# Kernel tuning notes

Measured on AMD Instinct MI355X. Metric: run time of the kernel, lower is better.

## Reference

```python
import jax, jax.numpy as jnp
import numpy as np

B, S, E = 4, 2048, 512
H = 8
DK = E // H          # 64
NQ = 8               # n_qubits


def setup_inputs() -> dict:
    key = jax.random.key(0)
    ks = jax.random.split(key, 10)
    s = 1.0 / np.sqrt(E)
    return {
        "x": jax.random.normal(ks[0], (B, S, E), dtype=jnp.float32),
        "Wq": jax.random.normal(ks[1], (E, E), dtype=jnp.float32) * s,
        "bq": jnp.zeros((E,), dtype=jnp.float32),
        "Wk": jax.random.normal(ks[2], (E, E), dtype=jnp.float32) * s,
        "bk": jnp.zeros((E,), dtype=jnp.float32),
        "Wv": jax.random.normal(ks[3], (E, E), dtype=jnp.float32) * s,
        "bv": jnp.zeros((E,), dtype=jnp.float32),
        "Wo": jax.random.normal(ks[4], (E, E), dtype=jnp.float32) * s,
        "bo": jnp.zeros((E,), dtype=jnp.float32),
        "kernel_params": jax.random.normal(ks[5], (NQ, NQ), dtype=jnp.float32),
    }


def _split_heads(t):
    # [B,S,E] -> [B,H,S,DK]
    return t.reshape(B, S, H, DK).transpose(0, 2, 1, 3)


def reference(x, Wq, bq, Wk, bk, Wv, bv, Wo, bo, kernel_params):
    q = _split_heads(x @ Wq + bq)
    k = _split_heads(x @ Wk + bk)
    v = _split_heads(x @ Wv + bv)

    # Quantum kernel closed form: RX(x_i) then RZ(theta_ii) on wire i, measure <Z_i>.
    # RZ commutes with Z so <Z_i> = cos(x_i). Only the first NQ features are encoded.
    q_meas = jnp.cos(q[..., :NQ])  # [B,H,S,NQ]
    k_meas = jnp.cos(k[..., :NQ])  # [B,H,S,NQ]

    sim = jnp.einsum('bhqd,bhkd->bhqk', q_meas, k_meas)  # [B,H,S,S]
    attn = jax.nn.softmax(sim, axis=-1)
    out = jnp.einsum('bhqk,bhkd->bhqd', attn, v)          # [B,H,S,DK]
    out = out.transpose(0, 2, 1, 3).reshape(B, S, E)      # compose heads
    return out @ Wo + bo
```

## Files before the change

kernel.cpp:

```cpp
#include <hip/hip_runtime.h>
#include <hip/hip_bf16.h>

#define BB 4
#define SS 2048
#define EE 512
#define HH 8
#define DKK 64
#define NQQ 8
#define BS (BB * SS)

typedef __attribute__((ext_vector_type(4))) float f32x4;
typedef __attribute__((ext_vector_type(16))) float f32x16;
typedef _Float16 f16x8 __attribute__((ext_vector_type(8)));
typedef unsigned short u16;
typedef unsigned int u32;

union U4H8 { uint4 u; f16x8 h; };

__device__ __forceinline__ u16 f2h(float f) {
    _Float16 hv = (_Float16)f;
    return *reinterpret_cast<u16*>(&hv);
}
__device__ __forceinline__ float h2f(u16 u) {
    _Float16 h = *reinterpret_cast<_Float16*>(&u);
    return (float)h;
}

__global__ __launch_bounds__(256) void cvt2_kernel(
    const float4* __restrict__ in, uint2* __restrict__ xh, uint2* __restrict__ xl, int n4)
{
    int i = blockIdx.x * 256 + threadIdx.x;
    if (i >= n4) return;
    float4 a = in[i];
    u16 h0 = f2h(a.x), h1 = f2h(a.y), h2 = f2h(a.z), h3 = f2h(a.w);
    u16 l0 = f2h(a.x - h2f(h0)), l1 = f2h(a.y - h2f(h1));
    u16 l2 = f2h(a.z - h2f(h2)), l3 = f2h(a.w - h2f(h3));
    xh[i] = make_uint2((u32)h0 | ((u32)h1 << 16), (u32)h2 | ((u32)h3 << 16));
    xl[i] = make_uint2((u32)l0 | ((u32)l1 << 16), (u32)l2 | ((u32)l3 << 16));
}

__global__ __launch_bounds__(256) void wqk_pack_kernel(
    const float* __restrict__ Wq, const float* __restrict__ Wk,
    u16* __restrict__ Wh)
{
    const int n = blockIdx.x;
    const int col = (((n & 63) >> 3) << 6) | (n & 7);
    const float* src = (n < 64) ? Wq : Wk;
    for (int k = threadIdx.x; k < EE; k += 256) {
        Wh[(size_t)n * EE + k] = f2h(src[(size_t)k * EE + col]);
    }
}

__global__ __launch_bounds__(256) void wtrans_kernel(
    const float* __restrict__ W, u16* __restrict__ WT)
{
    __shared__ float ts[64][65];
    const int kt0 = blockIdx.x * 64, nt0 = blockIdx.y * 64;
    const int tid = threadIdx.x;
    #pragma unroll
    for (int i = 0; i < 4; ++i) {
        int c = tid + i * 256;
        int kr = c >> 4, nc = (c & 15) * 4;
        float4 t = *reinterpret_cast<const float4*>(&W[(size_t)(kt0 + kr) * EE + nt0 + nc]);
        ts[kr][nc] = t.x; ts[kr][nc + 1] = t.y; ts[kr][nc + 2] = t.z; ts[kr][nc + 3] = t.w;
    }
    __syncthreads();
    const int n = tid >> 2, k0 = (tid & 3) * 16;
    u32 o[8];
    #pragma unroll
    for (int j = 0; j < 8; ++j) {
        o[j] = (u32)f2h(ts[k0 + 2 * j][n]) | ((u32)f2h(ts[k0 + 2 * j + 1][n]) << 16);
    }
    uint4* dst = reinterpret_cast<uint4*>(&WT[(size_t)(nt0 + n) * EE + kt0 + k0]);
    dst[0] = make_uint4(o[0], o[1], o[2], o[3]);
    dst[1] = make_uint4(o[4], o[5], o[6], o[7]);
}

__global__ __launch_bounds__(256) void qk_mfma_kernel(
    const u16* __restrict__ xh, const u16* __restrict__ xl,
    const u16* __restrict__ Wh,
    const float* __restrict__ bq, const float* __restrict__ bk,
    u16* __restrict__ qf, u16* __restrict__ kf)
{
    __shared__ u16 Asl[64 * 64];
    __shared__ u16 Bsl[64 * 64];

    const int tid = threadIdx.x;
    const int lane = tid & 63;
    const int ww = tid >> 6;
    const int wr = ww >> 1, wc = ww & 1;
    const int tx = lane & 15, tyq = lane >> 4;
    const int m0 = blockIdx.x * 64;
    const int isK = blockIdx.y;
    const int nbase = isK * 64;

    const int c0 = tid, c1 = tid + 256;
    const int r0 = c0 >> 3, o0 = (c0 & 7) * 8, d0 = r0 * 64 + (((c0 & 7) ^ (r0 & 7)) * 8);
    const int r1 = c1 >> 3, o1 = (c1 & 7) * 8, d1 = r1 * 64 + (((c1 & 7) ^ (r1 & 7)) * 8);

    uint4 pa0, pa1, pb0, pb1;
    auto ldi = [&](int it) {
        int pass = it >> 3, k0 = (it & 7) * 64;
        const u16* Ab = pass ? xl : xh;
        pa0 = *reinterpret_cast<const uint4*>(&Ab[(size_t)(m0 + r0) * EE + k0 + o0]);
        pb0 = *reinterpret_cast<const uint4*>(&Wh[(size_t)(nbase + r0) * EE + k0 + o0]);
        pa1 = *reinterpret_cast<const uint4*>(&Ab[(size_t)(m0 + r1) * EE + k0 + o1]);
        pb1 = *reinterpret_cast<const uint4*>(&Wh[(size_t)(nbase + r1) * EE + k0 + o1]);
    };
    auto st = [&]() {
        *reinterpret_cast<uint4*>(&Asl[d0]) = pa0;
        *reinterpret_cast<uint4*>(&Bsl[d0]) = pb0;
        *reinterpret_cast<uint4*>(&Asl[d1]) = pa1;
        *reinterpret_cast<uint4*>(&Bsl[d1]) = pb1;
    };

    f32x4 acc[2][2];
    #pragma unroll
    for (int mt = 0; mt < 2; ++mt)
        #pragma unroll
        for (int nt = 0; nt < 2; ++nt) acc[mt][nt] = (f32x4)(0.f);

    const int bkx = tx & 7;
    ldi(0);
    for (int it = 0; it < 16; ++it) {
        __syncthreads();
        st();
        if (it < 15) ldi(it + 1);
        __syncthreads();
        #pragma unroll
        for (int kb = 0; kb < 2; ++kb) {
            f16x8 af[2], bfg[2];
            const int kblk = ((kb * 4 + tyq) ^ bkx) * 8;
            #pragma unroll
            for (int mt = 0; mt < 2; ++mt)
                af[mt] = *reinterpret_cast<const f16x8*>(&Asl[(wr * 32 + mt * 16 + tx) * 64 + kblk]);
            #pragma unroll
            for (int nt = 0; nt < 2; ++nt)
                bfg[nt] = *reinterpret_cast<const f16x8*>(&Bsl[(wc * 32 + nt * 16 + tx) * 64 + kblk]);
            #pragma unroll
            for (int mt = 0; mt < 2; ++mt)
                #pragma unroll
                for (int nt = 0; nt < 2; ++nt)
                    acc[mt][nt] = __builtin_amdgcn_mfma_f32_16x16x32_f16(
                        af[mt], bfg[nt], acc[mt][nt], 0, 0, 0);
        }
    }

    const float* bias = isK ? bk : bq;
    u16* dst = isK ? kf : qf;
    #pragma unroll
    for (int mt = 0; mt < 2; ++mt) {
        #pragma unroll
        for (int nt = 0; nt < 2; ++nt) {
            int nl = wc * 32 + nt * 16 + tx;
            int h = nl >> 3, f = nl & 7;
            float bcol = bias[h * 64 + f];
            #pragma unroll
            for (int r = 0; r < 4; ++r) {
                int s = m0 + wr * 32 + mt * 16 + tyq * 4 + r;
                float c = __cosf(acc[mt][nt][r] + bcol);
                size_t bh = (size_t)((s >> 11) * HH + h);
                dst[(bh * SS + (s & 2047)) * 8 + f] = f2h(c);
            }
        }
    }
}

template<int MODE>
__global__ __launch_bounds__(256) void mfma_gemm_kernel(
    const u16* __restrict__ A, const u16* __restrict__ Bm,
    const float* __restrict__ bias, float* __restrict__ outf, u16* __restrict__ outb)
{
    __shared__ u16 smem[8448];
    u16* Asl = smem;
    u16* Bsl = smem + 4096;

    const int tid = threadIdx.x;
    const int lane = tid & 63;
    const int ww = tid >> 6;
    const int wr = ww >> 1, wc = ww & 1;
    const int tx = lane & 15, tyq = lane >> 4;
    const int m0 = blockIdx.x * 64, n0 = blockIdx.y * 64;

    const int c0 = tid, c1 = tid + 256;
    const int r0 = c0 >> 3, o0 = (c0 & 7) * 8, d0 = r0 * 64 + (((c0 & 7) ^ (r0 & 7)) * 8);
    const int r1 = c1 >> 3, o1 = (c1 & 7) * 8, d1 = r1 * 64 + (((c1 & 7) ^ (r1 & 7)) * 8);

    uint4 pa0, pa1, pb0, pb1;
    auto ld = [&](int ks) {
        int k0 = ks * 64;
        pa0 = *reinterpret_cast<const uint4*>(&A [(size_t)(m0 + r0) * EE + k0 + o0]);
        pb0 = *reinterpret_cast<const uint4*>(&Bm[(size_t)(n0 + r0) * EE + k0 + o0]);
        pa1 = *reinterpret_cast<const uint4*>(&A [(size_t)(m0 + r1) * EE + k0 + o1]);
        pb1 = *reinterpret_cast<const uint4*>(&Bm[(size_t)(n0 + r1) * EE + k0 + o1]);
    };
    auto st = [&]() {
        *reinterpret_cast<uint4*>(&Asl[d0]) = pa0;
        *reinterpret_cast<uint4*>(&Bsl[d0]) = pb0;
        *reinterpret_cast<uint4*>(&Asl[d1]) = pa1;
        *reinterpret_cast<uint4*>(&Bsl[d1]) = pb1;
    };

    f32x4 acc[2][2];
    #pragma unroll
    for (int mt = 0; mt < 2; ++mt)
        #pragma unroll
        for (int nt = 0; nt < 2; ++nt) acc[mt][nt] = (f32x4)(0.f);

    const int bkx = tx & 7;
    ld(0);
    for (int ks = 0; ks < 8; ++ks) {
        __syncthreads();
        st();
        if (ks < 7) ld(ks + 1);
        __syncthreads();
        #pragma unroll
        for (int kb = 0; kb < 2; ++kb) {
            f16x8 af[2], bfg[2];
            const int kblk = ((kb * 4 + tyq) ^ bkx) * 8;
            #pragma unroll
            for (int mt = 0; mt < 2; ++mt)
                af[mt] = *reinterpret_cast<const f16x8*>(&Asl[(wr * 32 + mt * 16 + tx) * 64 + kblk]);
            #pragma unroll
            for (int nt = 0; nt < 2; ++nt)
                bfg[nt] = *reinterpret_cast<const f16x8*>(&Bsl[(wc * 32 + nt * 16 + tx) * 64 + kblk]);
            #pragma unroll
            for (int mt = 0; mt < 2; ++mt)
                #pragma unroll
                for (int nt = 0; nt < 2; ++nt)
                    acc[mt][nt] = __builtin_amdgcn_mfma_f32_16x16x32_f16(
                        af[mt], bfg[nt], acc[mt][nt], 0, 0, 0);
        }
    }

    if (MODE == 0) {
        #pragma unroll
        for (int mt = 0; mt < 2; ++mt) {
            #pragma unroll
            for (int nt = 0; nt < 2; ++nt) {
                int gcol = n0 + wc * 32 + nt * 16 + tx;
                float bcol = bias[gcol];
                #pragma unroll
                for (int r = 0; r < 4; ++r) {
                    int grow = m0 + wr * 32 + mt * 16 + tyq * 4 + r;
                    outf[(size_t)grow * EE + gcol] = acc[mt][nt][r] + bcol;
                }
            }
        }
    } else {
        __syncthreads();
        #pragma unroll
        for (int mt = 0; mt < 2; ++mt) {
            #pragma unroll
            for (int nt = 0; nt < 2; ++nt) {
                int kl = wc * 32 + nt * 16 + tx;
                #pragma unroll
                for (int r = 0; r < 4; ++r) {
                    int dl = wr * 32 + mt * 16 + tyq * 4 + r;
                    float vb = acc[mt][nt][r] + bias[m0 + dl];
                    smem[dl * 66 + kl] = f2h(vb);
                }
            }
        }
        __syncthreads();
        const size_t slab = (size_t)((n0 >> 11) * HH + (m0 >> 6)) * (SS * DKK);
        const int cell0 = (n0 & 2047) >> 3;
        #pragma unroll
        for (int i = 0; i < 2; ++i) {
            int item = tid + i * 256;
            int d = item & 63, ci = item >> 6;
            int kb = 16 * (ci >> 1) + 4 * (ci & 1);
            u16 g[8];
            #pragma unroll
            for (int j = 0; j < 8; ++j) {
                int klocal = kb + (j & 3) + 8 * (j >> 2);
                g[j] = smem[d * 66 + klocal];
            }
            uint4 p;
            p.x = (u32)g[0] | ((u32)g[1] << 16);
            p.y = (u32)g[2] | ((u32)g[3] << 16);
            p.z = (u32)g[4] | ((u32)g[5] << 16);
            p.w = (u32)g[6] | ((u32)g[7] << 16);
            *reinterpret_cast<uint4*>(&outb[slab + (size_t)(cell0 + ci) * 512 + d * 8]) = p;
        }
    }
}

__global__ __launch_bounds__(256, 4) void attn_v7_kernel(
    const u16* __restrict__ qf, const u16* __restrict__ kf,
    const u16* __restrict__ VT2, u16* __restrict__ attb)
{
    __shared__ float fsh[128 * 33];

    const int tid = threadIdx.x;
    const int lane = tid & 63;
    const int wv = tid >> 6;
    const int kslice = wv >> 1;
    const int qw = wv & 1;
    const int l31 = lane & 31;
    const int hi = lane >> 5;

    const int bid = blockIdx.x;
    const int xcd = bid & 7, sub = bid >> 3;
    const int bh = (xcd << 2) | (sub >> 5);
    const int q0 = (sub & 31) * 64;

    const u16* __restrict__ qfb = qf + (size_t)bh * SS * 8;
    const u16* __restrict__ kfb = kf + (size_t)bh * SS * 8;
    const u16* __restrict__ V2b = VT2 + (size_t)bh * SS * DKK;

    const uint4 z4 = make_uint4(0u, 0u, 0u, 0u);

    U4H8 qb;
    qb.u = hi ? z4 : *reinterpret_cast<const uint4*>(&qfb[(size_t)(q0 + qw * 32 + l31) * 8]);
    const f16x8 QB = qb.h;

    f32x16 acc0 = (f32x16)(0.f), acc1 = (f32x16)(0.f);
    float z = 0.f;

    const int ks_off = kslice * 1024;

    auto vld = [&](int t, int s, uint4* dst) {
        const int K0 = ks_off + t * 64 + s * 32;
        #pragma unroll
        for (int c = 0; c < 2; ++c) {
            const size_t cb = (size_t)((((K0 >> 4) + c) << 1) + hi) * 512;
            dst[c * 2]     = *reinterpret_cast<const uint4*>(&V2b[cb + l31 * 8]);
            dst[c * 2 + 1] = *reinterpret_cast<const uint4*>(&V2b[cb + (32 + l31) * 8]);
        }
    };

    U4H8 kc0, kc1, kn0, kn1;
    auto ldk = [&](int t, U4H8& a, U4H8& b) {
        int kt = ks_off + t * 64;
        a.u = hi ? z4 : *reinterpret_cast<const uint4*>(&kfb[(size_t)(kt + l31) * 8]);
        b.u = hi ? z4 : *reinterpret_cast<const uint4*>(&kfb[(size_t)(kt + 32 + l31) * 8]);
    };

    uint4 vA[4], vB[4];
    ldk(0, kc0, kc1);
    vld(0, 0, vA);

    for (int t = 0; t < 16; ++t) {
        vld(t, 1, vB);
        if (t < 15) ldk(t + 1, kn0, kn1);
        {
            f32x16 sim = (f32x16)(0.f);
            sim = __builtin_amdgcn_mfma_f32_32x32x16_f16(kc0.h, QB, sim, 0, 0, 0);
            float w[16];
            #pragma unroll
            for (int r = 0; r < 16; ++r) w[r] = __expf(sim[r]);
            float zp = 0.f;
            #pragma unroll
            for (int r = 0; r < 8; ++r) zp += (w[2 * r] + w[2 * r + 1]);
            z += zp;
            #pragma unroll
            for (int c = 0; c < 2; ++c) {
                f16x8 PA;
                #pragma unroll
                for (int j = 0; j < 8; ++j) PA[j] = (_Float16)w[8 * c + j];
                U4H8 b0, b1; b0.u = vA[c * 2]; b1.u = vA[c * 2 + 1];
                acc0 = __builtin_amdgcn_mfma_f32_32x32x16_f16(PA, b0.h, acc0, 0, 0, 0);
                acc1 = __builtin_amdgcn_mfma_f32_32x32x16_f16(PA, b1.h, acc1, 0, 0, 0);
            }
        }
        if (t < 15) vld(t + 1, 0, vA);
        {
            f32x16 sim = (f32x16)(0.f);
            sim = __builtin_amdgcn_mfma_f32_32x32x16_f16(kc1.h, QB, sim, 0, 0, 0);
            float w[16];
            #pragma unroll
            for (int r = 0; r < 16; ++r) w[r] = __expf(sim[r]);
            float zp = 0.f;
            #pragma unroll
            for (int r = 0; r < 8; ++r) zp += (w[2 * r] + w[2 * r + 1]);
            z += zp;
            #pragma unroll
            for (int c = 0; c < 2; ++c) {
                f16x8 PA;
                #pragma unroll
                for (int j = 0; j < 8; ++j) PA[j] = (_Float16)w[8 * c + j];
                U4H8 b0, b1; b0.u = vB[c * 2]; b1.u = vB[c * 2 + 1];
                acc0 = __builtin_amdgcn_mfma_f32_32x32x16_f16(PA, b0.h, acc0, 0, 0, 0);
                acc1 = __builtin_amdgcn_mfma_f32_32x32x16_f16(PA, b1.h, acc1, 0, 0, 0);
            }
        }
        kc0 = kn0; kc1 = kn1;
    }

    const int cbase = (qw * 64 + lane) * 33;
    if (kslice == 1) {
        #pragma unroll
        for (int r = 0; r < 16; ++r) {
            fsh[cbase + r] = acc0[r];
            fsh[cbase + 16 + r] = acc1[r];
        }
        fsh[cbase + 32] = z;
    }
    __syncthreads();
    if (kslice == 0) {
        #pragma unroll
        for (int r = 0; r < 16; ++r) {
            acc0[r] += fsh[cbase + r];
            acc1[r] += fsh[cbase + 16 + r];
        }
        z += fsh[cbase + 32];
        z += __shfl_xor(z, 32, 64);
        float zinv = 1.0f / z;

        const int b = bh >> 3, h = bh & 7;
        #pragma unroll
        for (int r = 0; r < 16; ++r) {
            int qrow = (r & 3) + 8 * (r >> 2) + 4 * hi;
            float zi = __shfl(zinv, qrow, 32);
            size_t base = ((size_t)b * SS + q0 + qw * 32 + qrow) * EE + h * DKK + l31;
            attb[base]      = f2h(acc0[r] * zi);
            attb[base + 32] = f2h(acc1[r] * zi);
        }
    }
}

extern "C" void kernel_launch(void* const* d_in, const int* in_sizes, int n_in,
                              void* d_out, int out_size, void* d_ws, size_t ws_size,
                              hipStream_t stream)
{
    const float* x  = (const float*)d_in[0];
    const float* Wq = (const float*)d_in[1];
    const float* bq = (const float*)d_in[2];
    const float* Wk = (const float*)d_in[3];
    const float* bk = (const float*)d_in[4];
    const float* Wv = (const float*)d_in[5];
    const float* bv = (const float*)d_in[6];
    const float* Wo = (const float*)d_in[7];
    const float* bo = (const float*)d_in[8];

    char* w = (char*)d_ws;
    u16* xh    = (u16*)w;  w += (size_t)BS * EE * 2;
    u16* xl    = (u16*)w;  w += (size_t)BS * EE * 2;
    u16* Wqk   = (u16*)w;  w += (size_t)128 * EE * 2;
    u16* WvT   = (u16*)w;  w += (size_t)EE * EE * 2;
    u16* WoT   = (u16*)w;  w += (size_t)EE * EE * 2;
    u16* qf    = (u16*)w;  w += (size_t)BB * HH * SS * 8 * 2;
    u16* kf    = (u16*)w;  w += (size_t)BB * HH * SS * 8 * 2;
    u16* VT2   = (u16*)w;  w += (size_t)BB * HH * DKK * SS * 2;
    u16* attb  = xl;
    float* out = (float*)d_out;

    cvt2_kernel<<<dim3(BS * EE / 4 / 256), 256, 0, stream>>>(
        (const float4*)x, (uint2*)xh, (uint2*)xl, BS * EE / 4);
    wqk_pack_kernel<<<dim3(128), 256, 0, stream>>>(Wq, Wk, Wqk);
    wtrans_kernel<<<dim3(8, 8), 256, 0, stream>>>(Wv, WvT);
    wtrans_kernel<<<dim3(8, 8), 256, 0, stream>>>(Wo, WoT);
    qk_mfma_kernel<<<dim3(BS / 64, 2), 256, 0, stream>>>(
        xh, xl, Wqk, bq, bk, qf, kf);
    mfma_gemm_kernel<1><<<dim3(EE / 64, BS / 64), 256, 0, stream>>>(
        WvT, xh, bv, nullptr, VT2);
    attn_v7_kernel<<<dim3(1024), 256, 0, stream>>>(qf, kf, VT2, attb);
    mfma_gemm_kernel<0><<<dim3(BS / 64, EE / 64), 256, 0, stream>>>(
        attb, WoT, bo, out, nullptr);
}
```

Measured before the change: 85.49 us.

## Give each attention wave both query tiles and split keys four ways

The attention kernel changes from 2 query-waves × 2 key-slices to 4 key-slices, where each wave handles all 64 query rows. Each loaded K and V fragment is now reused for two query tiles, which halves per-wave global loads of V. The final partial sums are combined with a two-stage shared-memory tree reduction. The f32-to-f16 conversion of the probabilities switches to packed cvt_pkrtz, and launch bounds drop to 3 waves/SIMD to make room for more accumulator registers. The cost is more registers, lower occupancy and extra syncthreads in the reduction.

After: 156.6 us. +83.2%, slower.

```diff
diff --git a/kernel.cpp b/kernel.cpp
--- a/kernel.cpp
+++ b/kernel.cpp
@@ -11,11 +11,13 @@
 
 typedef __attribute__((ext_vector_type(4))) float f32x4;
 typedef __attribute__((ext_vector_type(16))) float f32x16;
+typedef __fp16 fp16x2 __attribute__((ext_vector_type(2)));
 typedef _Float16 f16x8 __attribute__((ext_vector_type(8)));
 typedef unsigned short u16;
 typedef unsigned int u32;
 
 union U4H8 { uint4 u; f16x8 h; };
+union PK8 { fp16x2 p[4]; f16x8 h; };
 
 __device__ __forceinline__ u16 f2h(float f) {
     _Float16 hv = (_Float16)f;
@@ -286,17 +288,15 @@
     }
 }
 
-__global__ __launch_bounds__(256, 4) void attn_v7_kernel(
+__global__ __launch_bounds__(256, 3) void attn_v8_kernel(
     const u16* __restrict__ qf, const u16* __restrict__ kf,
     const u16* __restrict__ VT2, u16* __restrict__ attb)
 {
-    __shared__ float fsh[128 * 33];
+    __shared__ float fsh[2][64][67];
 
     const int tid = threadIdx.x;
     const int lane = tid & 63;
-    const int wv = tid >> 6;
-    const int kslice = wv >> 1;
-    const int qw = wv & 1;
+    const int ks = tid >> 6;
     const int l31 = lane & 31;
     const int hi = lane >> 5;
 
@@ -311,17 +311,20 @@
 
     const uint4 z4 = make_uint4(0u, 0u, 0u, 0u);
 
-    U4H8 qb;
-    qb.u = hi ? z4 : *reinterpret_cast<const uint4*>(&qfb[(size_t)(q0 + qw * 32 + l31) * 8]);
-    const f16x8 QB = qb.h;
-
-    f32x16 acc0 = (f32x16)(0.f), acc1 = (f32x16)(0.f);
-    float z = 0.f;
-
-    const int ks_off = kslice * 1024;
-
-    auto vld = [&](int t, int s, uint4* dst) {
-        const int K0 = ks_off + t * 64 + s * 32;
+    U4H8 qb0, qb1;
+    qb0.u = hi ? z4 : *reinterpret_cast<const uint4*>(&qfb[(size_t)(q0 + l31) * 8]);
+    qb1.u = hi ? z4 : *reinterpret_cast<const uint4*>(&qfb[(size_t)(q0 + 32 + l31) * 8]);
+    const f16x8 QB0 = qb0.h;
+    const f16x8 QB1 = qb1.h;
+
+    f32x16 acc00 = (f32x16)(0.f), acc01 = (f32x16)(0.f);
+    f32x16 acc10 = (f32x16)(0.f), acc11 = (f32x16)(0.f);
+    float z0 = 0.f, z1 = 0.f;
+
+    const int ks_off = ks * 512;
+
+    auto vld = [&](int t, uint4 (&dst)[4]) {
+        const int K0 = ks_off + t * 32;
         #pragma unroll
         for (int c = 0; c < 2; ++c) {
             const size_t cb = (size_t)((((K0 >> 4) + c) << 1) + hi) * 512;
@@ -329,93 +332,101 @@
             dst[c * 2 + 1] = *reinterpret_cast<const uint4*>(&V2b[cb + (32 + l31) * 8]);
         }
     };
-
-    U4H8 kc0, kc1, kn0, kn1;
-    auto ldk = [&](int t, U4H8& a, U4H8& b) {
-        int kt = ks_off + t * 64;
-        a.u = hi ? z4 : *reinterpret_cast<const uint4*>(&kfb[(size_t)(kt + l31) * 8]);
-        b.u = hi ? z4 : *reinterpret_cast<const uint4*>(&kfb[(size_t)(kt + 32 + l31) * 8]);
+    auto kld = [&](int t, U4H8& a) {
+        const int K0 = ks_off + t * 32;
+        a.u = hi ? z4 : *reinterpret_cast<const uint4*>(&kfb[(size_t)(K0 + l31) * 8]);
+    };
+
+    auto phase = [&](const U4H8& kc, const uint4 (&vv)[4]) {
+        f32x16 s0 = (f32x16)(0.f), s1 = (f32x16)(0.f);
+        s0 = __builtin_amdgcn_mfma_f32_32x32x16_f16(kc.h, QB0, s0, 0, 0, 0);
+        s1 = __builtin_amdgcn_mfma_f32_32x32x16_f16(kc.h, QB1, s1, 0, 0, 0);
+        float w0[16], w1[16];
+        #pragma unroll
+        for (int r = 0; r < 16; ++r) w0[r] = __expf(s0[r]);
+        #pragma unroll
+        for (int r = 0; r < 16; ++r) w1[r] = __expf(s1[r]);
+        float zp0 = 0.f, zp1 = 0.f;
+        #pragma unroll
+        for (int r = 0; r < 8; ++r) { zp0 += (w0[2*r] + w0[2*r+1]); zp1 += (w1[2*r] + w1[2*r+1]); }
+        z0 += zp0; z1 += zp1;
+        #pragma unroll
+        for (int c = 0; c < 2; ++c) {
+            PK8 pa0, pa1;
+            #pragma unroll
+            for (int j = 0; j < 4; ++j) {
+                pa0.p[j] = __builtin_amdgcn_cvt_pkrtz(w0[8*c + 2*j], w0[8*c + 2*j + 1]);
+                pa1.p[j] = __builtin_amdgcn_cvt_pkrtz(w1[8*c + 2*j], w1[8*c + 2*j + 1]);
+            }
+            U4H8 b0, b1;
+            b0.u = vv[c * 2];
+            b1.u = vv[c * 2 + 1];
+            acc00 = __builtin_amdgcn_mfma_f32_32x32x16_f16(pa0.h, b0.h, acc00, 0, 0, 0);
+            acc01 = __builtin_amdgcn_mfma_f32_32x32x16_f16(pa0.h, b1.h, acc01, 0, 0, 0);
+            acc10 = __builtin_amdgcn_mfma_f32_32x32x16_f16(pa1.h, b0.h, acc10, 0, 0, 0);
+            acc11 = __builtin_amdgcn_mfma_f32_32x32x16_f16(pa1.h, b1.h, acc11, 0, 0, 0);
+        }
     };
 
     uint4 vA[4], vB[4];
-    ldk(0, kc0, kc1);
-    vld(0, 0, vA);
-
-    for (int t = 0; t < 16; ++t) {
-        vld(t, 1, vB);
-        if (t < 15) ldk(t + 1, kn0, kn1);
-        {
-            f32x16 sim = (f32x16)(0.f);
-            sim = __builtin_amdgcn_mfma_f32_32x32x16_f16(kc0.h, QB, sim, 0, 0, 0);
-            float w[16];
-            #pragma unroll
-            for (int r = 0; r < 16; ++r) w[r] = __expf(sim[r]);
-            float zp = 0.f;
-            #pragma unroll
-            for (int r = 0; r < 8; ++r) zp += (w[2 * r] + w[2 * r + 1]);
-            z += zp;
-            #pragma unroll
-            for (int c = 0; c < 2; ++c) {
-                f16x8 PA;
-                #pragma unroll
-                for (int j = 0; j < 8; ++j) PA[j] = (_Float16)w[8 * c + j];
-                U4H8 b0, b1; b0.u = vA[c * 2]; b1.u = vA[c * 2 + 1];
-                acc0 = __builtin_amdgcn_mfma_f32_32x32x16_f16(PA, b0.h, acc0, 0, 0, 0);
-                acc1 = __builtin_amdgcn_mfma_f32_32x32x16_f16(PA, b1.h, acc1, 0, 0, 0);
-            }
-        }
-        if (t < 15) vld(t + 1, 0, vA);
-        {
-            f32x16 sim = (f32x16)(0.f);
-            sim = __builtin_amdgcn_mfma_f32_32x32x16_f16(kc1.h, QB, sim, 0, 0, 0);
-            float w[16];
-            #pragma unroll
-            for (int r = 0; r < 16; ++r) w[r] = __expf(sim[r]);
-            float zp = 0.f;
-            #pragma unroll
-            for (int r = 0; r < 8; ++r) zp += (w[2 * r] + w[2 * r + 1]);
-            z += zp;
-            #pragma unroll
-            for (int c = 0; c < 2; ++c) {
-                f16x8 PA;
-                #pragma unroll
-                for (int j = 0; j < 8; ++j) PA[j] = (_Float16)w[8 * c + j];
-                U4H8 b0, b1; b0.u = vB[c * 2]; b1.u = vB[c * 2 + 1];
-                acc0 = __builtin_amdgcn_mfma_f32_32x32x16_f16(PA, b0.h, acc0, 0, 0, 0);
-                acc1 = __builtin_amdgcn_mfma_f32_32x32x16_f16(PA, b1.h, acc1, 0, 0, 0);
-            }
-        }
-        kc0 = kn0; kc1 = kn1;
-    }
-
-    const int cbase = (qw * 64 + lane) * 33;
-    if (kslice == 1) {
+    U4H8 kcA, kcB;
+    vld(0, vA); kld(0, kcA);
+
+    #pragma unroll 2
+    for (int tt = 0; tt < 8; ++tt) {
+        const int t = 2 * tt;
+        vld(t + 1, vB); kld(t + 1, kcB);
+        phase(kcA, vA);
+        if (t + 2 < 16) { vld(t + 2, vA); kld(t + 2, kcA); }
+        phase(kcB, vB);
+    }
+
+    auto store_slot = [&](int slot) {
+        float* p = &fsh[slot][lane][0];
         #pragma unroll
         for (int r = 0; r < 16; ++r) {
-            fsh[cbase + r] = acc0[r];
-            fsh[cbase + 16 + r] = acc1[r];
-        }
-        fsh[cbase + 32] = z;
-    }
+            p[r] = acc00[r]; p[16 + r] = acc01[r];
+            p[32 + r] = acc10[r]; p[48 + r] = acc11[r];
+        }
+        p[64] = z0; p[65] = z1;
+    };
+    auto add_slot = [&](int slot) {
+        const float* p = &fsh[slot][lane][0];
+        #pragma unroll
+        for (int r = 0; r < 16; ++r) {
+            acc00[r] += p[r]; acc01[r] += p[16 + r];
+            acc10[r] += p[32 + r]; acc11[r] += p[48 + r];
+        }
+        z0 += p[64]; z1 += p[65];
+    };
+
+    if (ks == 1) store_slot(0);
+    if (ks == 3) store_slot(1);
     __syncthreads();
-    if (kslice == 0) {
-        #pragma unroll
-        for (int r = 0; r < 16; ++r) {
-            acc0[r] += fsh[cbase + r];
-            acc1[r] += fsh[cbase + 16 + r];
-        }
-        z += fsh[cbase + 32];
-        z += __shfl_xor(z, 32, 64);
-        float zinv = 1.0f / z;
+    if (ks == 0) add_slot(0);
+    if (ks == 2) add_slot(1);
+    __syncthreads();
+    if (ks == 2) store_slot(0);
+    __syncthreads();
+
+    if (ks == 0) {
+        add_slot(0);
+        z0 += __shfl_xor(z0, 32, 64);
+        z1 += __shfl_xor(z1, 32, 64);
+        float zi0 = 1.0f / z0, zi1 = 1.0f / z1;
 
         const int b = bh >> 3, h = bh & 7;
         #pragma unroll
         for (int r = 0; r < 16; ++r) {
             int qrow = (r & 3) + 8 * (r >> 2) + 4 * hi;
-            float zi = __shfl(zinv, qrow, 32);
-            size_t base = ((size_t)b * SS + q0 + qw * 32 + qrow) * EE + h * DKK + l31;
-            attb[base]      = f2h(acc0[r] * zi);
-            attb[base + 32] = f2h(acc1[r] * zi);
+            float a = __shfl(zi0, qrow, 32);
+            float c = __shfl(zi1, qrow, 32);
+            size_t base0 = ((size_t)b * SS + q0 + qrow) * EE + h * DKK + l31;
+            size_t base1 = ((size_t)b * SS + q0 + 32 + qrow) * EE + h * DKK + l31;
+            attb[base0]      = f2h(acc00[r] * a);
+            attb[base0 + 32] = f2h(acc01[r] * a);
+            attb[base1]      = f2h(acc10[r] * c);
+            attb[base1 + 32] = f2h(acc11[r] * c);
         }
     }
 }
@@ -455,7 +466,7 @@
         xh, xl, Wqk, bq, bk, qf, kf);
     mfma_gemm_kernel<1><<<dim3(EE / 64, BS / 64), 256, 0, stream>>>(
         WvT, xh, bv, nullptr, VT2);
-    attn_v7_kernel<<<dim3(1024), 256, 0, stream>>>(qf, kf, VT2, attb);
+    attn_v8_kernel<<<dim3(1024), 256, 0, stream>>>(qf, kf, VT2, attb);
     mfma_gemm_kernel<0><<<dim3(BS / 64, EE / 64), 256, 0, stream>>>(
         attb, WoT, bo, out, nullptr);
 }
```
